# Optimization experiments

Measured on AMD Instinct MI355X. Metric: run time of the kernel, lower is better.

The kernel has to match this reference:

```python
import jax, jax.numpy as jnp
import numpy as np

EPS = 1e-5

def _block(x, W, b, g, be):
    # Linear -> LayerNorm -> ReLU, fused elementwise chain
    h = x @ W + b
    mu = jnp.mean(h, axis=-1, keepdims=True)
    var = jnp.mean(jnp.square(h - mu), axis=-1, keepdims=True)
    hn = (h - mu) * jax.lax.rsqrt(var + EPS) * g + be
    return jnp.maximum(hn, 0.0)

def setup_inputs() -> dict:
    key = jax.random.key(0)
    ks = jax.random.split(key, 6)
    B, D_IN, H, D_OUT = 262144, 48, 256, 12
    s_in = 1.0 / np.sqrt(D_IN)
    s_h = 1.0 / np.sqrt(H)
    return {
        "x": jax.random.normal(ks[0], (B, D_IN), jnp.float32),
        "W1": jax.random.normal(ks[1], (D_IN, H), jnp.float32) * s_in,
        "b1": jnp.zeros((H,), jnp.float32),
        "g1": jnp.ones((H,), jnp.float32),
        "be1": jnp.zeros((H,), jnp.float32),
        "W2": jax.random.normal(ks[2], (H, H), jnp.float32) * s_h,
        "b2": jnp.zeros((H,), jnp.float32),
        "g2": jnp.ones((H,), jnp.float32),
        "be2": jnp.zeros((H,), jnp.float32),
        "W3": jax.random.normal(ks[3], (H, H), jnp.float32) * s_h,
        "b3": jnp.zeros((H,), jnp.float32),
        "g3": jnp.ones((H,), jnp.float32),
        "be3": jnp.zeros((H,), jnp.float32),
        "Wm": jax.random.normal(ks[4], (H, D_OUT), jnp.float32) * s_h,
        "bm": jnp.zeros((D_OUT,), jnp.float32),
    }

def reference(x, W1, b1, g1, be1, W2, b2, g2, be2, W3, b3, g3, be3, Wm, bm):
    h = _block(x, W1, b1, g1, be1)
    h = _block(h, W2, b2, g2, be2)
    h = _block(h, W3, b3, g3, be3)
    return jnp.tanh(h @ Wm + bm)
```

## Files before the change

### kernel.cpp

```cpp
#include <hip/hip_runtime.h>
#include <hip/hip_bf16.h>

#define BATCH 262144
#define DIN 48
#define HDIM 256
#define DOUT 12
#define EPSV 1e-5f

#define ROWS_PER_BLOCK 128
#define NBLK (BATCH / ROWS_PER_BLOCK)

typedef __attribute__((ext_vector_type(4))) float f32x4;
typedef __attribute__((ext_vector_type(2))) float f32x2;
typedef __attribute__((ext_vector_type(8))) short bf16x8;

union FragU { bf16x8 v; unsigned u[4]; };

#define W1F_OFF 0
#define W2F_OFF 16384
#define W3F_OFF 81920
#define WMF_OFF 147456
#define WS_ELEMS 151552

#define WAITV(n) asm volatile("s_waitcnt vmcnt(" #n ")" ::: "memory")

__device__ __forceinline__ unsigned short f2b(float f) {
    union { float f; unsigned u; } v; v.f = f;
    unsigned r = (v.u + 0x7fffu + ((v.u >> 16) & 1u)) >> 16;
    return (unsigned short)r;
}

__device__ __forceinline__ unsigned packbf(float a, float b) {
    float2 t; t.x = a; t.y = b;
    __hip_bfloat162 h = __float22bfloat162_rn(t);
    union { __hip_bfloat162 h; unsigned u; } c; c.h = h;
    return c.u;
}

__device__ __forceinline__ float fast_tanh(float x) {
    const float t = __expf(2.0f * x);
    return fmaf(-2.0f, __builtin_amdgcn_rcpf(t + 1.0f), 1.0f);
}

__global__ void conv_w_kernel(const float* __restrict__ W1, const float* __restrict__ b1,
                              const float* __restrict__ W2, const float* __restrict__ W3,
                              const float* __restrict__ Wm,
                              unsigned short* __restrict__ ws) {
    int i = blockIdx.x * 256 + threadIdx.x;
    if (i >= WS_ELEMS) return;
    float v;
    if (i < W2F_OFF) {
        const int j = i & 7, l = (i >> 3) & 63, t = (i >> 9) & 15, s = i >> 13;
        const int n = 16 * t + (l & 15), k = 32 * s + 8 * (l >> 4) + j;
        v = (k < DIN) ? W1[k * HDIM + n] : (k == DIN ? b1[n] : 0.0f);
    } else if (i < W3F_OFF) {
        const int i2 = i - W2F_OFF;
        const int j = i2 & 7, l = (i2 >> 3) & 63, t = (i2 >> 9) & 15, s = i2 >> 13;
        const int n = 16 * t + (l & 15);
        const int k = 32 * s + ((j >= 4) ? 16 : 0) + 4 * (l >> 4) + (j & 3);
        v = W2[k * HDIM + n];
    } else if (i < WMF_OFF) {
        const int i3 = i - W3F_OFF;
        const int j = i3 & 7, l = (i3 >> 3) & 63, t = (i3 >> 9) & 15, s = i3 >> 13;
        const int n = 16 * t + (l & 15);
        const int k = 32 * s + ((j >= 4) ? 16 : 0) + 4 * (l >> 4) + (j & 3);
        v = W3[k * HDIM + n];
    } else {
        const int i4 = i - WMF_OFF;
        const int j = i4 & 7, l = (i4 >> 3) & 63, ks = i4 >> 9;
        const int n = l & 15;
        const int k = 32 * ks + ((j >= 4) ? 16 : 0) + 4 * (l >> 4) + (j & 3);
        v = (n < DOUT) ? Wm[k * DOUT + n] : 0.0f;
    }
    ws[i] = f2b(v);
}

__device__ __forceinline__ void gll16(const void* g, void* l) {
    __builtin_amdgcn_global_load_lds(
        (const __attribute__((address_space(1))) unsigned int*)g,
        (__attribute__((address_space(3))) unsigned int*)l, 16, 0, 0);
}

__device__ __forceinline__ void stage_half(const unsigned short* __restrict__ src,
                                           unsigned short* dst, int tid) {
    const char* g = (const char*)src + tid * 16;
    char* l = (char*)dst + tid * 16;
    gll16(g, l);
    gll16(g + 4096, l + 4096);
}

__device__ __forceinline__ void compute_slab(
    f32x4 (&acc)[2][16], const FragU& b0, const FragU& b1,
    const unsigned short* sb, const unsigned short* __restrict__ gw, int lane)
{
    bf16x8 AG[8];
    #pragma unroll
    for (int t = 0; t < 8; t++)
        AG[t] = *(const bf16x8*)&gw[(t * 64 + lane) * 8];
    __builtin_amdgcn_s_setprio(1);
    #pragma unroll
    for (int t = 0; t < 8; t++) {
        const bf16x8 A = *(const bf16x8*)&sb[(t * 64 + lane) * 8];
        acc[0][t] = __builtin_amdgcn_mfma_f32_16x16x32_bf16(A, b0.v, acc[0][t], 0, 0, 0);
        acc[1][t] = __builtin_amdgcn_mfma_f32_16x16x32_bf16(A, b1.v, acc[1][t], 0, 0, 0);
    }
    #pragma unroll
    for (int t = 0; t < 8; t++) {
        acc[0][8 + t] = __builtin_amdgcn_mfma_f32_16x16x32_bf16(AG[t], b0.v, acc[0][8 + t], 0, 0, 0);
        acc[1][8 + t] = __builtin_amdgcn_mfma_f32_16x16x32_bf16(AG[t], b1.v, acc[1][8 + t], 0, 0, 0);
    }
    __builtin_amdgcn_s_setprio(0);
}

#define SV2(v, a, b) __builtin_shufflevector(v, v, a, b)

__device__ __forceinline__ void build_frags(
    const f32x4 (&acc)[2][16], FragU (&bfo)[2][8],
    const float* __restrict__ gt, const float* __restrict__ bt, int lane)
{
    const int q4 = (lane >> 4) * 4;
    #pragma unroll
    for (int rt = 0; rt < 2; rt++) {
        f32x2 s2 = {0.f, 0.f}, p2 = {0.f, 0.f};
        #pragma unroll
        for (int t = 0; t < 16; t++) {
            const f32x2 a = SV2(acc[rt][t], 0, 1);
            const f32x2 b = SV2(acc[rt][t], 2, 3);
            s2 += a; s2 += b;
            p2 += a * a; p2 += b * b;
        }
        float ss = s2[0] + s2[1];
        float qq = p2[0] + p2[1];
        ss += __shfl_xor(ss, 16); ss += __shfl_xor(ss, 32);
        qq += __shfl_xor(qq, 16); qq += __shfl_xor(qq, 32);
        const float mu = ss * (1.0f / 256.0f);
        const float rs = __builtin_amdgcn_rsqf(
            fmaxf(qq * (1.0f / 256.0f) - mu * mu, 0.0f) + EPSV);
        const float nb = -mu * rs;
        const f32x2 rs2 = {rs, rs}, nb2 = {nb, nb}, z2 = {0.f, 0.f};
        #pragma unroll
        for (int ks = 0; ks < 8; ks++) {
            const f32x4 g0 = *(const f32x4*)&gt[32 * ks + q4];
            const f32x4 e0 = *(const f32x4*)&bt[32 * ks + q4];
            const f32x4 g1 = *(const f32x4*)&gt[32 * ks + 16 + q4];
            const f32x4 e1 = *(const f32x4*)&bt[32 * ks + 16 + q4];
            const f32x2 v00 = SV2(acc[rt][2 * ks], 0, 1);
            const f32x2 v01 = SV2(acc[rt][2 * ks], 2, 3);
            const f32x2 v10 = SV2(acc[rt][2 * ks + 1], 0, 1);
            const f32x2 v11 = SV2(acc[rt][2 * ks + 1], 2, 3);
            const f32x2 w00 = __builtin_elementwise_max(
                (v00 * rs2 + nb2) * SV2(g0, 0, 1) + SV2(e0, 0, 1), z2);
            const f32x2 w01 = __builtin_elementwise_max(
                (v01 * rs2 + nb2) * SV2(g0, 2, 3) + SV2(e0, 2, 3), z2);
            const f32x2 w10 = __builtin_elementwise_max(
                (v10 * rs2 + nb2) * SV2(g1, 0, 1) + SV2(e1, 0, 1), z2);
            const f32x2 w11 = __builtin_elementwise_max(
                (v11 * rs2 + nb2) * SV2(g1, 2, 3) + SV2(e1, 2, 3), z2);
            bfo[rt][ks].u[0] = packbf(w00[0], w00[1]);
            bfo[rt][ks].u[1] = packbf(w01[0], w01[1]);
            bfo[rt][ks].u[2] = packbf(w10[0], w10[1]);
            bfo[rt][ks].u[3] = packbf(w11[0], w11[1]);
        }
    }
}

__device__ __forceinline__ void zero_acc(f32x4 (&acc)[2][16]) {
    #pragma unroll
    for (int rt = 0; rt < 2; rt++)
        #pragma unroll
        for (int t = 0; t < 16; t++)
            acc[rt][t] = (f32x4){0.f, 0.f, 0.f, 0.f};
}

__device__ __forceinline__ void init_acc_bias(f32x4 (&acc)[2][16],
                                              const float* __restrict__ bt, int q) {
    #pragma unroll
    for (int t = 0; t < 16; t++) {
        const f32x4 b = *(const f32x4*)&bt[16 * t + 4 * q];
        acc[0][t] = b;
        acc[1][t] = b;
    }
}

__global__ __launch_bounds__(256, 2) void fused_mlp(
    const float* __restrict__ x,
    const float* __restrict__ g1, const float* __restrict__ be1,
    const float* __restrict__ b2, const float* __restrict__ g2, const float* __restrict__ be2,
    const float* __restrict__ b3, const float* __restrict__ g3, const float* __restrict__ be3,
    const float* __restrict__ bm,
    const unsigned short* __restrict__ ws,
    float* __restrict__ out)
{
    __shared__ unsigned short buf[4][4096];
    __shared__ float gtab[3][256];
    __shared__ float betab[3][256];
    __shared__ float btab[2][256];
    __shared__ float bmt[16];
    __shared__ float ostage[4][384];

    const int tid = threadIdx.x;
    const int wv = tid >> 6, lane = tid & 63;
    const int l15 = lane & 15, q = lane >> 4;
    const int wrow0 = blockIdx.x * ROWS_PER_BLOCK + wv * 32;

    const unsigned short* w1f = ws + W1F_OFF;
    const unsigned short* w2f = ws + W2F_OFF;
    const unsigned short* w3f = ws + W3F_OFF;
    const unsigned short* wmf = ws + WMF_OFF;

    stage_half(w1f, &buf[0][0], tid);
    stage_half(w1f + 8192, &buf[1][0], tid);

    {
        const int n = tid;
        gtab[0][n] = g1[n];  betab[0][n] = be1[n];
        gtab[1][n] = g2[n];  betab[1][n] = be2[n];
        gtab[2][n] = g3[n];  betab[2][n] = be3[n];
        btab[0][n] = b2[n];
        btab[1][n] = b3[n];
        if (tid < 16) bmt[tid] = (tid < DOUT) ? bm[tid] : 0.f;
    }
    FragU bf[2][8];
    #pragma unroll
    for (int rt = 0; rt < 2; rt++) {
        const float* xr = x + (size_t)(wrow0 + rt * 16 + l15) * DIN;
        const float4 f0 = *(const float4*)(xr + q * 8);
        const float4 f1 = *(const float4*)(xr + q * 8 + 4);
        bf[rt][0].u[0] = packbf(f0.x, f0.y); bf[rt][0].u[1] = packbf(f0.z, f0.w);
        bf[rt][0].u[2] = packbf(f1.x, f1.y); bf[rt][0].u[3] = packbf(f1.z, f1.w);
        if (q < 2) {
            const float4 f2 = *(const float4*)(xr + 32 + q * 8);
            const float4 f3 = *(const float4*)(xr + 36 + q * 8);
            bf[rt][1].u[0] = packbf(f2.x, f2.y); bf[rt][1].u[1] = packbf(f2.z, f2.w);
            bf[rt][1].u[2] = packbf(f3.x, f3.y); bf[rt][1].u[3] = packbf(f3.z, f3.w);
        } else if (q == 2) {
            bf[rt][1].u[0] = 0x00003F80u;
            bf[rt][1].u[1] = 0u; bf[rt][1].u[2] = 0u; bf[rt][1].u[3] = 0u;
        } else {
            bf[rt][1].u[0] = 0u; bf[rt][1].u[1] = 0u;
            bf[rt][1].u[2] = 0u; bf[rt][1].u[3] = 0u;
        }
    }
    asm volatile("s_waitcnt lgkmcnt(0)" ::: "memory");

    f32x4 acc[2][16];


    zero_acc(acc);
    #pragma unroll
    for (int s = 0; s < 2; s++) {
        stage_half(w2f + s * 8192, &buf[(s + 2) & 3][0], tid);
        WAITV(4);
        __builtin_amdgcn_s_barrier();
        __builtin_amdgcn_sched_barrier(0);
        compute_slab(acc, bf[0][s], bf[1][s], &buf[s][0],
                     w1f + s * 8192 + 4096, lane);
    }
    build_frags(acc, bf, &gtab[0][0], &betab[0][0], lane);

    init_acc_bias(acc, &btab[0][0], q);
    #pragma unroll
    for (int s = 0; s < 8; s++) {
        const unsigned short* nsrc = (s < 6) ? (w2f + (s + 2) * 8192)
                                             : (w3f + (s - 6) * 8192);
        stage_half(nsrc, &buf[(s + 4) & 3][0], tid);
        WAITV(4);
        __builtin_amdgcn_s_barrier();
        __builtin_amdgcn_sched_barrier(0);
        compute_slab(acc, bf[0][s], bf[1][s], &buf[(s + 2) & 3][0],
                     w2f + s * 8192 + 4096, lane);
    }
    build_frags(acc, bf, &gtab[1][0], &betab[1][0], lane);

    init_acc_bias(acc, &btab[1][0], q);
    #pragma unroll
    for (int s = 0; s < 8; s++) {
        if (s < 6) stage_half(w3f + (s + 2) * 8192, &buf[(s + 12) & 3][0], tid);
        if (s < 6)      { WAITV(4); }
        else if (s == 6){ WAITV(2); }
        else            { WAITV(0); }
        __builtin_amdgcn_s_barrier();
        __builtin_amdgcn_sched_barrier(0);
        compute_slab(acc, bf[0][s], bf[1][s], &buf[(s + 10) & 3][0],
                     w3f + s * 8192 + 4096, lane);
    }
    build_frags(acc, bf, &gtab[2][0], &betab[2][0], lane);

    f32x4 facc[2];
    {
        const f32x4 bm4 = *(const f32x4*)&bmt[4 * q];
        facc[0] = bm4;
        facc[1] = bm4;
    }
    #pragma unroll
    for (int ks = 0; ks < 8; ks++) {
        const bf16x8 A = *(const bf16x8*)&wmf[(ks * 64 + lane) * 8];
        facc[0] = __builtin_amdgcn_mfma_f32_16x16x32_bf16(A, bf[0][ks].v, facc[0], 0, 0, 0);
        facc[1] = __builtin_amdgcn_mfma_f32_16x16x32_bf16(A, bf[1][ks].v, facc[1], 0, 0, 0);
    }
    if (q < 3) {
        #pragma unroll
        for (int rt = 0; rt < 2; rt++) {
            float4 o;
            o.x = fast_tanh(facc[rt][0]);
            o.y = fast_tanh(facc[rt][1]);
            o.z = fast_tanh(facc[rt][2]);
            o.w = fast_tanh(facc[rt][3]);
            *(float4*)&ostage[wv][(rt * 16 + l15) * 12 + q * 4] = o;
        }
    }
    float4* og = (float4*)(out + (size_t)wrow0 * DOUT);
    const float4* ov = (const float4*)&ostage[wv][0];
    og[lane] = ov[lane];
    if (lane < 32) og[64 + lane] = ov[64 + lane];
}

extern "C" void kernel_launch(void* const* d_in, const int* in_sizes, int n_in,
                              void* d_out, int out_size, void* d_ws, size_t ws_size,
                              hipStream_t stream)
{
    const float* x   = (const float*)d_in[0];
    const float* W1  = (const float*)d_in[1];
    const float* b1  = (const float*)d_in[2];
    const float* g1  = (const float*)d_in[3];
    const float* be1 = (const float*)d_in[4];
    const float* W2  = (const float*)d_in[5];
    const float* b2  = (const float*)d_in[6];
    const float* g2  = (const float*)d_in[7];
    const float* be2 = (const float*)d_in[8];
    const float* W3  = (const float*)d_in[9];
    const float* b3  = (const float*)d_in[10];
    const float* g3  = (const float*)d_in[11];
    const float* be3 = (const float*)d_in[12];
    const float* Wm  = (const float*)d_in[13];
    const float* bm  = (const float*)d_in[14];
    unsigned short* ws = (unsigned short*)d_ws;
    float* out = (float*)d_out;

    conv_w_kernel<<<(WS_ELEMS + 255) / 256, 256, 0, stream>>>(W1, b1, W2, W3, Wm, ws);
    fused_mlp<<<NBLK, 256, 0, stream>>>(x, g1, be1, b2, g2, be2,
                                        b3, g3, be3, bm, ws, out);
}
```

Before: 107.5 us.

## Halve block to two waves, prefetch global weight halves before LDS staging, drop LDS param tables

Shrinks each block from 4 waves and 128 rows to 2 waves and 64 rows, so each thread now stages four 16-byte chunks per weight slab. The direct global loads of the second half of each slab are hoisted ahead of the LDS staging, and the vmcnt waits are recounted for the larger number of loads in flight. The LayerNorm gamma/beta/bias tables in LDS are removed and read straight from global memory instead. This aims to cut LDS use and barrier cost and to overlap weight fetches with MFMA work. The trade-off is twice as many blocks, each re-reading all the weights, plus scattered global reads of small parameters.

```diff
diff --git a/kernel.cpp b/kernel.cpp
--- a/kernel.cpp
+++ b/kernel.cpp
@@ -7,7 +7,7 @@
 #define DOUT 12
 #define EPSV 1e-5f
 
-#define ROWS_PER_BLOCK 128
+#define ROWS_PER_BLOCK 64
 #define NBLK (BATCH / ROWS_PER_BLOCK)
 
 typedef __attribute__((ext_vector_type(4))) float f32x4;
@@ -85,18 +85,15 @@
                                            unsigned short* dst, int tid) {
     const char* g = (const char*)src + tid * 16;
     char* l = (char*)dst + tid * 16;
-    gll16(g, l);
-    gll16(g + 4096, l + 4096);
+    #pragma unroll
+    for (int c = 0; c < 4; c++)
+        gll16(g + c * 2048, l + c * 2048);
 }
 
 __device__ __forceinline__ void compute_slab(
     f32x4 (&acc)[2][16], const FragU& b0, const FragU& b1,
-    const unsigned short* sb, const unsigned short* __restrict__ gw, int lane)
+    const unsigned short* sb, const bf16x8 (&AG)[8], int lane)
 {
-    bf16x8 AG[8];
-    #pragma unroll
-    for (int t = 0; t < 8; t++)
-        AG[t] = *(const bf16x8*)&gw[(t * 64 + lane) * 8];
     __builtin_amdgcn_s_setprio(1);
     #pragma unroll
     for (int t = 0; t < 8; t++) {
@@ -182,7 +179,7 @@
     }
 }
 
-__global__ __launch_bounds__(256, 2) void fused_mlp(
+__global__ __launch_bounds__(128, 2) void fused_mlp(
     const float* __restrict__ x,
     const float* __restrict__ g1, const float* __restrict__ be1,
     const float* __restrict__ b2, const float* __restrict__ g2, const float* __restrict__ be2,
@@ -192,11 +189,7 @@
     float* __restrict__ out)
 {
     __shared__ unsigned short buf[4][4096];
-    __shared__ float gtab[3][256];
-    __shared__ float betab[3][256];
-    __shared__ float btab[2][256];
-    __shared__ float bmt[16];
-    __shared__ float ostage[4][384];
+    __shared__ float ostage[2][384];
 
     const int tid = threadIdx.x;
     const int wv = tid >> 6, lane = tid & 63;
@@ -211,15 +204,6 @@
     stage_half(w1f, &buf[0][0], tid);
     stage_half(w1f + 8192, &buf[1][0], tid);
 
-    {
-        const int n = tid;
-        gtab[0][n] = g1[n];  betab[0][n] = be1[n];
-        gtab[1][n] = g2[n];  betab[1][n] = be2[n];
-        gtab[2][n] = g3[n];  betab[2][n] = be3[n];
-        btab[0][n] = b2[n];
-        btab[1][n] = b3[n];
-        if (tid < 16) bmt[tid] = (tid < DOUT) ? bm[tid] : 0.f;
-    }
     FragU bf[2][8];
     #pragma unroll
     for (int rt = 0; rt < 2; rt++) {
@@ -241,7 +225,6 @@
             bf[rt][1].u[2] = 0u; bf[rt][1].u[3] = 0u;
         }
     }
-    asm volatile("s_waitcnt lgkmcnt(0)" ::: "memory");
 
     f32x4 acc[2][16];
 
@@ -249,46 +232,62 @@
     zero_acc(acc);
     #pragma unroll
     for (int s = 0; s < 2; s++) {
+        const unsigned short* sl = w1f + s * 8192;
+        bf16x8 AG[8];
+        #pragma unroll
+        for (int t = 0; t < 8; t++)
+            AG[t] = *(const bf16x8*)&sl[4096 + (t * 64 + lane) * 8];
+        __builtin_amdgcn_sched_barrier(0);
         stage_half(w2f + s * 8192, &buf[(s + 2) & 3][0], tid);
-        WAITV(4);
+        if (s == 0) { WAITV(16); } else { WAITV(24); }
         __builtin_amdgcn_s_barrier();
         __builtin_amdgcn_sched_barrier(0);
-        compute_slab(acc, bf[0][s], bf[1][s], &buf[s][0],
-                     w1f + s * 8192 + 4096, lane);
-    }
-    build_frags(acc, bf, &gtab[0][0], &betab[0][0], lane);
-
-    init_acc_bias(acc, &btab[0][0], q);
+        compute_slab(acc, bf[0][s], bf[1][s], &buf[s & 3][0], AG, lane);
+    }
+    build_frags(acc, bf, g1, be1, lane);
+
+    init_acc_bias(acc, b2, q);
     #pragma unroll
     for (int s = 0; s < 8; s++) {
+        const unsigned short* sl = w2f + s * 8192;
+        bf16x8 AG[8];
+        #pragma unroll
+        for (int t = 0; t < 8; t++)
+            AG[t] = *(const bf16x8*)&sl[4096 + (t * 64 + lane) * 8];
+        __builtin_amdgcn_sched_barrier(0);
         const unsigned short* nsrc = (s < 6) ? (w2f + (s + 2) * 8192)
                                              : (w3f + (s - 6) * 8192);
-        stage_half(nsrc, &buf[(s + 4) & 3][0], tid);
-        WAITV(4);
+        stage_half(nsrc, &buf[s & 3][0], tid);
+        WAITV(24);
         __builtin_amdgcn_s_barrier();
         __builtin_amdgcn_sched_barrier(0);
-        compute_slab(acc, bf[0][s], bf[1][s], &buf[(s + 2) & 3][0],
-                     w2f + s * 8192 + 4096, lane);
-    }
-    build_frags(acc, bf, &gtab[1][0], &betab[1][0], lane);
-
-    init_acc_bias(acc, &btab[1][0], q);
+        compute_slab(acc, bf[0][s], bf[1][s], &buf[(s + 2) & 3][0], AG, lane);
+    }
+    build_frags(acc, bf, g2, be2, lane);
+
+    init_acc_bias(acc, b3, q);
     #pragma unroll
     for (int s = 0; s < 8; s++) {
-        if (s < 6) stage_half(w3f + (s + 2) * 8192, &buf[(s + 12) & 3][0], tid);
-        if (s < 6)      { WAITV(4); }
-        else if (s == 6){ WAITV(2); }
-        else            { WAITV(0); }
+        const unsigned short* sl = w3f + s * 8192;
+        bf16x8 AG[8];
+        #pragma unroll
+        for (int t = 0; t < 8; t++)
+            AG[t] = *(const bf16x8*)&sl[4096 + (t * 64 + lane) * 8];
+        __builtin_amdgcn_sched_barrier(0);
+        if (s < 6) stage_half(w3f + (s + 2) * 8192, &buf[s & 3][0], tid);
+        if (s < 6)      { WAITV(24); }
+        else if (s == 6){ WAITV(20); }
+        else            { WAITV(16); }
         __builtin_amdgcn_s_barrier();
         __builtin_amdgcn_sched_barrier(0);
-        compute_slab(acc, bf[0][s], bf[1][s], &buf[(s + 10) & 3][0],
-                     w3f + s * 8192 + 4096, lane);
-    }
-    build_frags(acc, bf, &gtab[2][0], &betab[2][0], lane);
+        compute_slab(acc, bf[0][s], bf[1][s], &buf[(s + 2) & 3][0], AG, lane);
+    }
+    build_frags(acc, bf, g3, be3, lane);
 
     f32x4 facc[2];
     {
-        const f32x4 bm4 = *(const f32x4*)&bmt[4 * q];
+        f32x4 bm4 = {0.f, 0.f, 0.f, 0.f};
+        if (q < 3) bm4 = *(const f32x4*)&bm[4 * q];
         facc[0] = bm4;
         facc[1] = bm4;
     }
@@ -338,6 +337,6 @@
     float* out = (float*)d_out;
 
     conv_w_kernel<<<(WS_ELEMS + 255) / 256, 256, 0, stream>>>(W1, b1, W2, W3, Wm, ws);
-    fused_mlp<<<NBLK, 256, 0, stream>>>(x, g1, be1, b2, g2, be2,
+    fused_mlp<<<NBLK, 128, 0, stream>>>(x, g1, be1, b2, g2, be2,
                                         b3, g3, be3, bm, ws, out);
 }
```

New measurement: 142.7 us. +32.8%, slower.
